# Kernel optimization log

Hardware: AMD Instinct MI355X
Metric: run time of the kernel (lower is better)

## Reference

```python
import jax, jax.numpy as jnp
import numpy as np

B, T, C, H = 4, 2048, 1024, 16
HD = C // H  # head dim = 64


def setup_inputs() -> dict:
    key = jax.random.key(0)
    ks = jax.random.split(key, 8)
    s = 1.0 / np.sqrt(C)
    return {
        "x": jax.random.normal(ks[0], (B, T, C), dtype=jnp.float32),
        "Wq": jax.random.normal(ks[1], (C, C), dtype=jnp.float32) * s,
        "bq": jax.random.normal(ks[2], (C,), dtype=jnp.float32) * 0.02,
        "Wk": jax.random.normal(ks[3], (C, C), dtype=jnp.float32) * s,
        "bk": jax.random.normal(ks[4], (C,), dtype=jnp.float32) * 0.02,
        "Wv": jax.random.normal(ks[5], (C, C), dtype=jnp.float32) * s,
        "bv": jax.random.normal(ks[6], (C,), dtype=jnp.float32) * 0.02,
        "Wp": jax.random.normal(ks[7], (C, C), dtype=jnp.float32) * s,
    }


def reference(x, Wq, bq, Wk, bk, Wv, bv, Wp):
    # Separate Q/K/V projections (torch Linear: y = x @ W.T + b)
    q = jnp.einsum("btc,dc->btd", x, Wq) + bq
    k = jnp.einsum("btc,dc->btd", x, Wk) + bk
    v = jnp.einsum("btc,dc->btd", x, Wv) + bv
    # split heads -> [B, H, T, HD]
    q = q.reshape(B, T, H, HD).transpose(0, 2, 1, 3)
    k = k.reshape(B, T, H, HD).transpose(0, 2, 1, 3)
    v = v.reshape(B, T, H, HD).transpose(0, 2, 1, 3)
    # causal scaled dot-product attention
    scale = 1.0 / np.sqrt(HD)
    scores = jnp.einsum("bhqd,bhkd->bhqk", q, k) * scale
    causal_mask = jnp.tril(jnp.ones((T, T), dtype=bool))  # [T, T]
    scores = jnp.where(causal_mask, scores, jnp.finfo(scores.dtype).min)
    att = jax.nn.softmax(scores, axis=-1)
    y = jnp.einsum("bhqk,bhkd->bhqd", att, v)
    # merge heads and output projection (no bias)
    y = y.transpose(0, 2, 1, 3).reshape(B, T, C)
    return jnp.einsum("btc,dc->btd", y, Wp)
```

## Files before the change

### kernel.cpp

```cpp
#include <hip/hip_runtime.h>
#include <stdint.h>


typedef unsigned short u16;
typedef short bf16x8 __attribute__((ext_vector_type(8)));
typedef float f32x4  __attribute__((ext_vector_type(4)));

#define LOG2E 1.4426950408889634f
#define CSHIFT 8.0f

__device__ __forceinline__ void gload_lds16(const void* g, void* l) {
  __builtin_amdgcn_global_load_lds(
      (const __attribute__((address_space(1))) void*)g,
      (__attribute__((address_space(3))) void*)l,
      16, 0, 0);
}

__device__ __forceinline__ u16 f2bf(float f) {
  union { float f; uint32_t u; } v; v.f = f;
  uint32_t u = v.u;
  u += 0x7fffu + ((u >> 16) & 1u);
  return (u16)(u >> 16);
}

__device__ __forceinline__ uint32_t pack_bf16(float a, float b) {
#if __has_builtin(__builtin_amdgcn_cvt_pk_bf16_f32)
  typedef short v2s __attribute__((ext_vector_type(2)));
  v2s r = __builtin_amdgcn_cvt_pk_bf16_f32(a, b);
  union { v2s s; uint32_t u; } c; c.s = r;
  return c.u;
#else
  return (uint32_t)f2bf(a) | ((uint32_t)f2bf(b) << 16);
#endif
}

__device__ __forceinline__ float fexp2(float x) {
#if __has_builtin(__builtin_amdgcn_exp2f)
  return __builtin_amdgcn_exp2f(x);
#else
  return exp2f(x);
#endif
}

__global__ void cvt_all_kernel(const float* __restrict__ x,
                               const float* __restrict__ w0,
                               const float* __restrict__ w1,
                               const float* __restrict__ w2,
                               const float* __restrict__ w3,
                               uint4* __restrict__ out) {
  int i = blockIdx.x * blockDim.x + threadIdx.x;
  if (i >= 1572864) return;
  const float* src;
  int local;
  if (i < 1048576) { src = x; local = i; }
  else {
    int j = i - 1048576;
    int seg = j >> 17;
    local = j & 131071;
    src = (seg == 0) ? w0 : (seg == 1) ? w1 : (seg == 2) ? w2 : w3;
  }
  const int blk = local >> 9, s = local & 511;
  const int tile = blk >> 5, ks = blk & 31;
  const int r = s >> 6, ln = s & 63;
  const int row = tile * 128 + r * 16 + (ln & 15);
  const int col = ks * 32 + (ln >> 4) * 8;
  const float4* p = (const float4*)(src + (size_t)row * 1024 + col);
  const float4 v0 = p[0], v1 = p[1];
  uint4 pk;
  pk.x = pack_bf16(v0.x, v0.y); pk.y = pack_bf16(v0.z, v0.w);
  pk.z = pack_bf16(v1.x, v1.y); pk.w = pack_bf16(v1.z, v1.w);
  out[i] = pk;
}

__global__ __launch_bounds__(256, 3) void gemm_qkv(
    const u16* __restrict__ A,
    const u16* __restrict__ Wq, const u16* __restrict__ Wk, const u16* __restrict__ Wv,
    const float* __restrict__ bq, const float* __restrict__ bk, const float* __restrict__ bv,
    u16* __restrict__ Qo, u16* __restrict__ Ko, u16* __restrict__ Vo) {
  __shared__ __attribute__((aligned(16))) u16 ldsA[3][4096];
  __shared__ __attribute__((aligned(16))) u16 ldsB[3][4096];
  const int tid = threadIdx.x;
  const int wv = tid >> 6, lane = tid & 63;
  const int cl = lane & 15, quad = lane >> 4;
  const int m0 = blockIdx.x * 128;
  const int mat = blockIdx.y >> 3;
  const int nt0 = blockIdx.y & 7;
  const int n0 = nt0 * 128;
  const int wm = (wv >> 1) * 64, wn = (wv & 1) * 64;
  const u16* W = (mat == 0) ? Wq : (mat == 1) ? Wk : Wv;
  const float* bias = (mat == 0) ? bq : (mat == 1) ? bk : bv;

  const u16* Abase = A + ((size_t)blockIdx.x << 17);
  const u16* Wbase = W + ((size_t)nt0 << 17);

  auto stage = [&](int buf, int ks) {
    const u16* a = Abase + ((size_t)ks << 12);
    const u16* w = Wbase + ((size_t)ks << 12);
    gload_lds16(a + tid * 8,        &ldsA[buf][tid * 8]);
    gload_lds16(a + 2048 + tid * 8, &ldsA[buf][2048 + tid * 8]);
    gload_lds16(w + tid * 8,        &ldsB[buf][tid * 8]);
    gload_lds16(w + 2048 + tid * 8, &ldsB[buf][2048 + tid * 8]);
  };

  f32x4 acc[4][4] = {};

  stage(0, 0);
  stage(1, 1);

  for (int kt = 0; kt < 32; ++kt) {
    if (kt < 31) {
      asm volatile("s_waitcnt vmcnt(4)" ::: "memory");
    } else {
      asm volatile("s_waitcnt vmcnt(0)" ::: "memory");
    }
    __builtin_amdgcn_s_barrier();
    if (kt < 30) stage((kt + 2) % 3, kt + 2);
    const int buf = kt % 3;
    bf16x8 af[4], bfr[4];
#pragma unroll
    for (int i = 0; i < 4; i++)
      af[i] = *(const bf16x8*)&ldsA[buf][(((wm >> 4) + i) * 64 + lane) * 8];
#pragma unroll
    for (int j = 0; j < 4; j++)
      bfr[j] = *(const bf16x8*)&ldsB[buf][(((wn >> 4) + j) * 64 + lane) * 8];
#pragma unroll
    for (int i = 0; i < 4; i++)
#pragma unroll
      for (int j = 0; j < 4; j++)
        acc[i][j] = __builtin_amdgcn_mfma_f32_16x16x32_bf16(af[i], bfr[j], acc[i][j], 0, 0, 0);
  }

  if (mat == 2) {
#pragma unroll
    for (int j = 0; j < 4; j++) {
      const int n = n0 + wn + j * 16 + cl;
      const float bj = bias[n];
      const int h = n >> 6, hd = n & 63;
#pragma unroll
      for (int i = 0; i < 4; i++) {
        const int m = m0 + wm + i * 16 + quad * 4;
        const int b = m >> 11, t = m & 2047;
        uint2 pk;
        pk.x = pack_bf16(acc[i][j][0] + bj, acc[i][j][1] + bj);
        pk.y = pack_bf16(acc[i][j][2] + bj, acc[i][j][3] + bj);
        const size_t off = ((size_t)(b * 16 + h) << 17) + ((size_t)(t >> 7) << 13)
                         + (size_t)(((hd >> 4) * 4 + ((t >> 5) & 3)) * 512
                                    + (((t >> 3) & 3) * 16 + (hd & 15)) * 8 + (t & 7));
        *(uint2*)(Vo + off) = pk;
      }
    }
  } else if (mat == 1) {
#pragma unroll
    for (int j = 0; j < 4; j++) {
      const int n = n0 + wn + j * 16 + cl;
      const float bj = bias[n];
      const int h = n >> 6, hd = n & 63;
      const int rlo = hd >> 5, lhi = ((hd >> 3) & 3) * 16, e = hd & 7;
#pragma unroll
      for (int i = 0; i < 4; i++) {
#pragma unroll
        for (int r = 0; r < 4; r++) {
          const int m = m0 + wm + i * 16 + quad * 4 + r;
          const int b = m >> 11, t = m & 2047;
          const size_t off = ((size_t)(b * 16 + h) << 17) + ((size_t)(t >> 7) << 13)
                           + (size_t)(((((t >> 4) & 7) * 2 + rlo) * 512)
                                      + (lhi + (t & 15)) * 8 + e);
          Ko[off] = f2bf(acc[i][j][r] + bj);
        }
      }
    }
  } else {
    const float sc = 0.125f * LOG2E;
#pragma unroll
    for (int j = 0; j < 4; j++) {
      const int n = n0 + wn + j * 16 + cl;
      const float bj = bias[n];
      const int h = n >> 6, hd = n & 63;
#pragma unroll
      for (int i = 0; i < 4; i++) {
#pragma unroll
        for (int r = 0; r < 4; r++) {
          const int m = m0 + wm + i * 16 + quad * 4 + r;
          const int b = m >> 11, t = m & 2047;
          Qo[((size_t)(b * 16 + h) * 2048 + t) * 64 + hd] = f2bf((acc[i][j][r] + bj) * sc);
        }
      }
    }
  }
}

__global__ __launch_bounds__(256, 3) void gemm_out(
    const u16* __restrict__ A, const u16* __restrict__ W,
    float* __restrict__ out) {
  __shared__ __attribute__((aligned(16))) u16 ldsA[3][4096];
  __shared__ __attribute__((aligned(16))) u16 ldsB[3][4096];
  const int tid = threadIdx.x;
  const int wv = tid >> 6, lane = tid & 63;
  const int cl = lane & 15, quad = lane >> 4;
  const int m0 = blockIdx.x * 128;
  const int n0 = blockIdx.y * 128;
  const int wm = (wv >> 1) * 64, wn = (wv & 1) * 64;

  const u16* Abase = A + ((size_t)blockIdx.x << 17);
  const u16* Wbase = W + ((size_t)blockIdx.y << 17);

  auto stage = [&](int buf, int ks) {
    const u16* a = Abase + ((size_t)ks << 12);
    const u16* w = Wbase + ((size_t)ks << 12);
    gload_lds16(a + tid * 8,        &ldsA[buf][tid * 8]);
    gload_lds16(a + 2048 + tid * 8, &ldsA[buf][2048 + tid * 8]);
    gload_lds16(w + tid * 8,        &ldsB[buf][tid * 8]);
    gload_lds16(w + 2048 + tid * 8, &ldsB[buf][2048 + tid * 8]);
  };

  f32x4 acc[4][4] = {};

  stage(0, 0);
  stage(1, 1);

  for (int kt = 0; kt < 32; ++kt) {
    if (kt < 31) {
      asm volatile("s_waitcnt vmcnt(4)" ::: "memory");
    } else {
      asm volatile("s_waitcnt vmcnt(0)" ::: "memory");
    }
    __builtin_amdgcn_s_barrier();
    if (kt < 30) stage((kt + 2) % 3, kt + 2);
    const int buf = kt % 3;
    bf16x8 af[4], bfr[4];
#pragma unroll
    for (int i = 0; i < 4; i++)
      af[i] = *(const bf16x8*)&ldsA[buf][(((wm >> 4) + i) * 64 + lane) * 8];
#pragma unroll
    for (int j = 0; j < 4; j++)
      bfr[j] = *(const bf16x8*)&ldsB[buf][(((wn >> 4) + j) * 64 + lane) * 8];
#pragma unroll
    for (int i = 0; i < 4; i++)
#pragma unroll
      for (int j = 0; j < 4; j++)
        acc[i][j] = __builtin_amdgcn_mfma_f32_16x16x32_bf16(af[i], bfr[j], acc[i][j], 0, 0, 0);
  }

#pragma unroll
  for (int j = 0; j < 4; j++) {
    const int n = n0 + wn + j * 16 + cl;
#pragma unroll
    for (int i = 0; i < 4; i++)
#pragma unroll
      for (int r = 0; r < 4; r++) {
        const int m = m0 + wm + i * 16 + quad * 4 + r;
        out[(size_t)m * 1024 + n] = acc[i][j][r];
      }
  }
}

__global__ __launch_bounds__(256, 2) void attn_kernel(
    const u16* __restrict__ Qb, const u16* __restrict__ Kb,
    const u16* __restrict__ Vtb, u16* __restrict__ Yb) {
  __shared__ __attribute__((aligned(16))) u16 ldsK[2][8192];
  __shared__ __attribute__((aligned(16))) u16 ldsV[8192];
  __shared__ __attribute__((aligned(16))) u16 ldsP[4][32][128];
  const int tid = threadIdx.x;
  const int wv = tid >> 6, lane = tid & 63;
  const int cl = lane & 15, quad = lane >> 4;
  const int p = blockIdx.x + (blockIdx.y << 3);
  const int xcd = p & 7, l = p >> 3;
  const int bh = xcd * 8 + (l & 7);
  const int qtb = l >> 3;
  const int qhi = 15 - qtb, qlo = qtb;
  const u16* Qh = Qb + (size_t)bh * 2048 * 64;
  const u16* Kh = Kb + ((size_t)bh << 17);
  const u16* Vh = Vtb + ((size_t)bh << 17);

  bf16x8 qf[2][2][2];
#pragma unroll
  for (int t = 0; t < 2; ++t) {
    const int q0 = (t == 0 ? qhi : qlo) * 128;
#pragma unroll
    for (int rt = 0; rt < 2; ++rt)
#pragma unroll
      for (int ks = 0; ks < 2; ++ks)
        qf[t][rt][ks] = *(const bf16x8*)&Qh[(size_t)(q0 + wv * 32 + rt * 16 + cl) * 64 + ks * 32 + quad * 8];
  }

  f32x4 o[2][2][4] = {};
  float ls[2][2] = {};

  auto stageK = [&](int buf, int kt) {
    const u16* kb2 = Kh + ((size_t)kt << 13);
#pragma unroll
    for (int rep = 0; rep < 4; ++rep)
      gload_lds16(kb2 + (rep * 256 + tid) * 8, &ldsK[buf][(rep * 256 + tid) * 8]);
  };
  auto stageV = [&](int kt) {
    const u16* vb2 = Vh + ((size_t)kt << 13);
#pragma unroll
    for (int rep = 0; rep < 4; ++rep)
      gload_lds16(vb2 + (rep * 256 + tid) * 8, &ldsV[(rep * 256 + tid) * 8]);
  };

  stageK(0, 0);

  for (int kt = 0; kt <= qhi; ++kt) {
    const int buf = kt & 1;
    const bool dolo = (kt <= qlo);
    __syncthreads();

    stageV(kt);

#pragma unroll
    for (int ct = 0; ct < 8; ++ct) {
      const bf16x8 kf0 = *(const bf16x8*)&ldsK[buf][((ct * 2 + 0) * 64 + lane) * 8];
      const bf16x8 kf1 = *(const bf16x8*)&ldsK[buf][((ct * 2 + 1) * 64 + lane) * 8];
#pragma unroll
      for (int rt = 0; rt < 2; ++rt) {
        f32x4 s = {};
        s = __builtin_amdgcn_mfma_f32_16x16x32_bf16(kf0, qf[0][rt][0], s, 0, 0, 0);
        s = __builtin_amdgcn_mfma_f32_16x16x32_bf16(kf1, qf[0][rt][1], s, 0, 0, 0);
        float pv[4];
#pragma unroll
        for (int r = 0; r < 4; ++r) {
          pv[r] = fexp2(s[r] - CSHIFT);
          if (kt == qhi) {
            if (ct * 16 + quad * 4 + r > wv * 32 + rt * 16 + cl) pv[r] = 0.f;
          }
          ls[0][rt] += pv[r];
        }
        const int rl = rt * 16 + cl;
        const int swch = (2 * ct + (quad >> 1)) ^ (cl & 7);
        uint2 pw;
        pw.x = pack_bf16(pv[0], pv[1]);
        pw.y = pack_bf16(pv[2], pv[3]);
        *(uint2*)&ldsP[wv][rl][(swch << 3) + (quad & 1) * 4] = pw;
      }
    }

    __syncthreads();

    if (kt < qhi) stageK(1 - buf, kt + 1);

#pragma unroll
    for (int ks = 0; ks < 4; ++ks) {
      bf16x8 pf[2];
#pragma unroll
      for (int rt = 0; rt < 2; ++rt)
        pf[rt] = *(const bf16x8*)&ldsP[wv][rt * 16 + cl][(((4 * ks + quad) ^ (cl & 7)) << 3)];
#pragma unroll
      for (int nt = 0; nt < 4; ++nt) {
        const bf16x8 vf = *(const bf16x8*)&ldsV[((nt * 4 + ks) * 64 + lane) * 8];
        o[0][0][nt] = __builtin_amdgcn_mfma_f32_16x16x32_bf16(pf[0], vf, o[0][0][nt], 0, 0, 0);
        o[0][1][nt] = __builtin_amdgcn_mfma_f32_16x16x32_bf16(pf[1], vf, o[0][1][nt], 0, 0, 0);
      }
    }

    if (dolo) {
#pragma unroll
      for (int ct = 0; ct < 8; ++ct) {
        const bf16x8 kf0 = *(const bf16x8*)&ldsK[buf][((ct * 2 + 0) * 64 + lane) * 8];
        const bf16x8 kf1 = *(const bf16x8*)&ldsK[buf][((ct * 2 + 1) * 64 + lane) * 8];
#pragma unroll
        for (int rt = 0; rt < 2; ++rt) {
          f32x4 s = {};
          s = __builtin_amdgcn_mfma_f32_16x16x32_bf16(kf0, qf[1][rt][0], s, 0, 0, 0);
          s = __builtin_amdgcn_mfma_f32_16x16x32_bf16(kf1, qf[1][rt][1], s, 0, 0, 0);
          float pv[4];
#pragma unroll
          for (int r = 0; r < 4; ++r) {
            pv[r] = fexp2(s[r] - CSHIFT);
            if (kt == qlo) {
              if (ct * 16 + quad * 4 + r > wv * 32 + rt * 16 + cl) pv[r] = 0.f;
            }
            ls[1][rt] += pv[r];
          }
          const int rl = rt * 16 + cl;
          const int swch = (2 * ct + (quad >> 1)) ^ (cl & 7);
          uint2 pw;
          pw.x = pack_bf16(pv[0], pv[1]);
          pw.y = pack_bf16(pv[2], pv[3]);
          *(uint2*)&ldsP[wv][rl][(swch << 3) + (quad & 1) * 4] = pw;
        }
      }
#pragma unroll
      for (int ks = 0; ks < 4; ++ks) {
        bf16x8 pf[2];
#pragma unroll
        for (int rt = 0; rt < 2; ++rt)
          pf[rt] = *(const bf16x8*)&ldsP[wv][rt * 16 + cl][(((4 * ks + quad) ^ (cl & 7)) << 3)];
#pragma unroll
        for (int nt = 0; nt < 4; ++nt) {
          const bf16x8 vf = *(const bf16x8*)&ldsV[((nt * 4 + ks) * 64 + lane) * 8];
          o[1][0][nt] = __builtin_amdgcn_mfma_f32_16x16x32_bf16(pf[0], vf, o[1][0][nt], 0, 0, 0);
          o[1][1][nt] = __builtin_amdgcn_mfma_f32_16x16x32_bf16(pf[1], vf, o[1][1][nt], 0, 0, 0);
        }
      }
    }
  }

  const int bb = bh >> 4, h = bh & 15;
#pragma unroll
  for (int t = 0; t < 2; ++t) {
    const int q0 = (t == 0 ? qhi : qlo) * 128;
#pragma unroll
    for (int rt = 0; rt < 2; ++rt) {
      float s = ls[t][rt];
      s += __shfl_xor(s, 16, 64);
      s += __shfl_xor(s, 32, 64);
#pragma unroll
      for (int r = 0; r < 4; ++r) {
        const float inv = 1.0f / __shfl(s, quad * 4 + r, 64);
        const int q = q0 + wv * 32 + rt * 16 + quad * 4 + r;
        const int row = bb * 2048 + q;
#pragma unroll
        for (int nt = 0; nt < 4; ++nt) {
          const int col = h * 64 + nt * 16 + cl;
          const size_t off = ((size_t)((row >> 7) * 32 + (col >> 5)) << 12)
                           + (size_t)((((row >> 4) & 7) * 64 + ((col >> 3) & 3) * 16 + (row & 15)) * 8
                                      + (col & 7));
          Yb[off] = f2bf(o[t][rt][nt][r] * inv);
        }
      }
    }
  }
}

extern "C" void kernel_launch(void* const* d_in, const int* in_sizes, int n_in,
                              void* d_out, int out_size, void* d_ws, size_t ws_size,
                              hipStream_t stream) {
  const float* x  = (const float*)d_in[0];
  const float* Wq = (const float*)d_in[1];
  const float* bq = (const float*)d_in[2];
  const float* Wk = (const float*)d_in[3];
  const float* bk = (const float*)d_in[4];
  const float* Wv = (const float*)d_in[5];
  const float* bv = (const float*)d_in[6];
  const float* Wp = (const float*)d_in[7];

  u16* xb  = (u16*)d_ws;
  u16* wqb = xb  + 8388608;
  u16* wkb = wqb + 1048576;
  u16* wvb = wkb + 1048576;
  u16* wpb = wvb + 1048576;
  u16* Qb  = wpb + 1048576;
  u16* Kb  = Qb  + 8388608;
  u16* Vtb = Kb  + 8388608;
  u16* Yb  = Vtb + 8388608;

  cvt_all_kernel<<<6144, 256, 0, stream>>>(x, Wq, Wk, Wv, Wp, (uint4*)d_ws);

  gemm_qkv<<<dim3(64, 24), 256, 0, stream>>>(xb, wqb, wkb, wvb, bq, bk, bv,
                                             Qb, Kb, Vtb);

  attn_kernel<<<dim3(8, 64), 256, 0, stream>>>(Qb, Kb, Vtb, Yb);

  gemm_out<<<dim3(64, 8), 256, 0, stream>>>(Yb, wpb, (float*)d_out);
}
```

Before: 246.5 us.

## Stage GEMM epilogues through LDS and compute softmax row sums via MFMA

The QKV and output GEMM epilogues now write accumulators into a reused shared-memory tile and then emit coalesced 16-byte global stores, replacing scattered 2- and 4-byte stores. In attention, the per-lane softmax denominator accumulation and cross-lane shuffles are replaced by an extra MFMA against a ones vector, with a fast reciprocal for the final normalization. This trades extra LDS traffic, barriers and MFMA work for fewer VALU ops and better store coalescing.

```diff
diff --git a/kernel.cpp b/kernel.cpp
--- a/kernel.cpp
+++ b/kernel.cpp
@@ -39,6 +39,14 @@
   return __builtin_amdgcn_exp2f(x);
 #else
   return exp2f(x);
+#endif
+}
+
+__device__ __forceinline__ float frcp(float x) {
+#if __has_builtin(__builtin_amdgcn_rcpf)
+  return __builtin_amdgcn_rcpf(x);
+#else
+  return 1.0f / x;
 #endif
 }
 
@@ -77,8 +85,7 @@
     const u16* __restrict__ Wq, const u16* __restrict__ Wk, const u16* __restrict__ Wv,
     const float* __restrict__ bq, const float* __restrict__ bk, const float* __restrict__ bv,
     u16* __restrict__ Qo, u16* __restrict__ Ko, u16* __restrict__ Vo) {
-  __shared__ __attribute__((aligned(16))) u16 ldsA[3][4096];
-  __shared__ __attribute__((aligned(16))) u16 ldsB[3][4096];
+  __shared__ __attribute__((aligned(16))) u16 shm[24576];
   const int tid = threadIdx.x;
   const int wv = tid >> 6, lane = tid & 63;
   const int cl = lane & 15, quad = lane >> 4;
@@ -96,10 +103,12 @@
   auto stage = [&](int buf, int ks) {
     const u16* a = Abase + ((size_t)ks << 12);
     const u16* w = Wbase + ((size_t)ks << 12);
-    gload_lds16(a + tid * 8,        &ldsA[buf][tid * 8]);
-    gload_lds16(a + 2048 + tid * 8, &ldsA[buf][2048 + tid * 8]);
-    gload_lds16(w + tid * 8,        &ldsB[buf][tid * 8]);
-    gload_lds16(w + 2048 + tid * 8, &ldsB[buf][2048 + tid * 8]);
+    u16* la = &shm[buf * 4096];
+    u16* lb = &shm[12288 + buf * 4096];
+    gload_lds16(a + tid * 8,        la + tid * 8);
+    gload_lds16(a + 2048 + tid * 8, la + 2048 + tid * 8);
+    gload_lds16(w + tid * 8,        lb + tid * 8);
+    gload_lds16(w + 2048 + tid * 8, lb + 2048 + tid * 8);
   };
 
   f32x4 acc[4][4] = {};
@@ -116,13 +125,15 @@
     __builtin_amdgcn_s_barrier();
     if (kt < 30) stage((kt + 2) % 3, kt + 2);
     const int buf = kt % 3;
+    const u16* la = &shm[buf * 4096];
+    const u16* lb = &shm[12288 + buf * 4096];
     bf16x8 af[4], bfr[4];
 #pragma unroll
     for (int i = 0; i < 4; i++)
-      af[i] = *(const bf16x8*)&ldsA[buf][(((wm >> 4) + i) * 64 + lane) * 8];
+      af[i] = *(const bf16x8*)&la[(((wm >> 4) + i) * 64 + lane) * 8];
 #pragma unroll
     for (int j = 0; j < 4; j++)
-      bfr[j] = *(const bf16x8*)&ldsB[buf][(((wn >> 4) + j) * 64 + lane) * 8];
+      bfr[j] = *(const bf16x8*)&lb[(((wn >> 4) + j) * 64 + lane) * 8];
 #pragma unroll
     for (int i = 0; i < 4; i++)
 #pragma unroll
@@ -130,42 +141,40 @@
         acc[i][j] = __builtin_amdgcn_mfma_f32_16x16x32_bf16(af[i], bfr[j], acc[i][j], 0, 0, 0);
   }
 
+  __syncthreads();
+  u16* etile = shm;
+
   if (mat == 2) {
 #pragma unroll
     for (int j = 0; j < 4; j++) {
-      const int n = n0 + wn + j * 16 + cl;
-      const float bj = bias[n];
-      const int h = n >> 6, hd = n & 63;
+      const int n_loc = wn + j * 16 + cl;
+      const float bj = bias[n0 + n_loc];
+      const int hh = n_loc >> 6, hd = n_loc & 63;
 #pragma unroll
       for (int i = 0; i < 4; i++) {
-        const int m = m0 + wm + i * 16 + quad * 4;
-        const int b = m >> 11, t = m & 2047;
+        const int tb = wm + i * 16 + quad * 4;
         uint2 pk;
         pk.x = pack_bf16(acc[i][j][0] + bj, acc[i][j][1] + bj);
         pk.y = pack_bf16(acc[i][j][2] + bj, acc[i][j][3] + bj);
-        const size_t off = ((size_t)(b * 16 + h) << 17) + ((size_t)(t >> 7) << 13)
-                         + (size_t)(((hd >> 4) * 4 + ((t >> 5) & 3)) * 512
-                                    + (((t >> 3) & 3) * 16 + (hd & 15)) * 8 + (t & 7));
-        *(uint2*)(Vo + off) = pk;
+        const int off = ((hd >> 4) * 4 + ((tb >> 5) & 3)) * 512
+                      + (((tb >> 3) & 3) * 16 + (hd & 15)) * 8 + (tb & 7);
+        *(uint2*)&etile[hh * 8192 + off] = pk;
       }
     }
   } else if (mat == 1) {
 #pragma unroll
     for (int j = 0; j < 4; j++) {
-      const int n = n0 + wn + j * 16 + cl;
-      const float bj = bias[n];
-      const int h = n >> 6, hd = n & 63;
+      const int n_loc = wn + j * 16 + cl;
+      const float bj = bias[n0 + n_loc];
+      const int hh = n_loc >> 6, hd = n_loc & 63;
       const int rlo = hd >> 5, lhi = ((hd >> 3) & 3) * 16, e = hd & 7;
 #pragma unroll
       for (int i = 0; i < 4; i++) {
 #pragma unroll
         for (int r = 0; r < 4; r++) {
-          const int m = m0 + wm + i * 16 + quad * 4 + r;
-          const int b = m >> 11, t = m & 2047;
-          const size_t off = ((size_t)(b * 16 + h) << 17) + ((size_t)(t >> 7) << 13)
-                           + (size_t)(((((t >> 4) & 7) * 2 + rlo) * 512)
-                                      + (lhi + (t & 15)) * 8 + e);
-          Ko[off] = f2bf(acc[i][j][r] + bj);
+          const int tl = wm + i * 16 + quad * 4 + r;
+          const int off = (((tl >> 4) & 7) * 2 + rlo) * 512 + (lhi + (tl & 15)) * 8 + e;
+          etile[hh * 8192 + off] = f2bf(acc[i][j][r] + bj);
         }
       }
     }
@@ -173,18 +182,40 @@
     const float sc = 0.125f * LOG2E;
 #pragma unroll
     for (int j = 0; j < 4; j++) {
-      const int n = n0 + wn + j * 16 + cl;
-      const float bj = bias[n];
-      const int h = n >> 6, hd = n & 63;
+      const int n_loc = wn + j * 16 + cl;
+      const float bj = bias[n0 + n_loc];
+      const int hh = n_loc >> 6, hd = n_loc & 63;
 #pragma unroll
       for (int i = 0; i < 4; i++) {
 #pragma unroll
         for (int r = 0; r < 4; r++) {
-          const int m = m0 + wm + i * 16 + quad * 4 + r;
-          const int b = m >> 11, t = m & 2047;
-          Qo[((size_t)(b * 16 + h) * 2048 + t) * 64 + hd] = f2bf((acc[i][j][r] + bj) * sc);
+          const int tl = wm + i * 16 + quad * 4 + r;
+          etile[hh * 8192 + tl * 64 + hd] = f2bf((acc[i][j][r] + bj) * sc);
         }
       }
+    }
+  }
+  __syncthreads();
+
+  const int b = m0 >> 11, t0 = m0 & 2047;
+  const int h0 = n0 >> 6;
+  if (mat == 0) {
+#pragma unroll
+    for (int p = 0; p < 8; ++p) {
+      const int idx = p * 2048 + tid * 8;
+      const int hh = idx >> 13, off = idx & 8191;
+      u16* dst = Qo + ((size_t)(b * 16 + h0 + hh) * 2048 + t0) * 64 + off;
+      *(uint4*)dst = *(const uint4*)&etile[idx];
+    }
+  } else {
+    u16* base = (mat == 1) ? Ko : Vo;
+    const int kt = t0 >> 7;
+#pragma unroll
+    for (int p = 0; p < 8; ++p) {
+      const int idx = p * 2048 + tid * 8;
+      const int hh = idx >> 13, off = idx & 8191;
+      u16* dst = base + ((size_t)(b * 16 + h0 + hh) << 17) + ((size_t)kt << 13) + off;
+      *(uint4*)dst = *(const uint4*)&etile[idx];
     }
   }
 }
@@ -192,8 +223,7 @@
 __global__ __launch_bounds__(256, 3) void gemm_out(
     const u16* __restrict__ A, const u16* __restrict__ W,
     float* __restrict__ out) {
-  __shared__ __attribute__((aligned(16))) u16 ldsA[3][4096];
-  __shared__ __attribute__((aligned(16))) u16 ldsB[3][4096];
+  __shared__ __attribute__((aligned(16))) u16 shm[24576];
   const int tid = threadIdx.x;
   const int wv = tid >> 6, lane = tid & 63;
   const int cl = lane & 15, quad = lane >> 4;
@@ -207,10 +237,12 @@
   auto stage = [&](int buf, int ks) {
     const u16* a = Abase + ((size_t)ks << 12);
     const u16* w = Wbase + ((size_t)ks << 12);
-    gload_lds16(a + tid * 8,        &ldsA[buf][tid * 8]);
-    gload_lds16(a + 2048 + tid * 8, &ldsA[buf][2048 + tid * 8]);
-    gload_lds16(w + tid * 8,        &ldsB[buf][tid * 8]);
-    gload_lds16(w + 2048 + tid * 8, &ldsB[buf][2048 + tid * 8]);
+    u16* la = &shm[buf * 4096];
+    u16* lb = &shm[12288 + buf * 4096];
+    gload_lds16(a + tid * 8,        la + tid * 8);
+    gload_lds16(a + 2048 + tid * 8, la + 2048 + tid * 8);
+    gload_lds16(w + tid * 8,        lb + tid * 8);
+    gload_lds16(w + 2048 + tid * 8, lb + 2048 + tid * 8);
   };
 
   f32x4 acc[4][4] = {};
@@ -227,13 +259,15 @@
     __builtin_amdgcn_s_barrier();
     if (kt < 30) stage((kt + 2) % 3, kt + 2);
     const int buf = kt % 3;
+    const u16* la = &shm[buf * 4096];
+    const u16* lb = &shm[12288 + buf * 4096];
     bf16x8 af[4], bfr[4];
 #pragma unroll
     for (int i = 0; i < 4; i++)
-      af[i] = *(const bf16x8*)&ldsA[buf][(((wm >> 4) + i) * 64 + lane) * 8];
+      af[i] = *(const bf16x8*)&la[(((wm >> 4) + i) * 64 + lane) * 8];
 #pragma unroll
     for (int j = 0; j < 4; j++)
-      bfr[j] = *(const bf16x8*)&ldsB[buf][(((wn >> 4) + j) * 64 + lane) * 8];
+      bfr[j] = *(const bf16x8*)&lb[(((wn >> 4) + j) * 64 + lane) * 8];
 #pragma unroll
     for (int i = 0; i < 4; i++)
 #pragma unroll
@@ -241,16 +275,33 @@
         acc[i][j] = __builtin_amdgcn_mfma_f32_16x16x32_bf16(af[i], bfr[j], acc[i][j], 0, 0, 0);
   }
 
-#pragma unroll
-  for (int j = 0; j < 4; j++) {
-    const int n = n0 + wn + j * 16 + cl;
-#pragma unroll
-    for (int i = 0; i < 4; i++)
-#pragma unroll
-      for (int r = 0; r < 4; r++) {
-        const int m = m0 + wm + i * 16 + quad * 4 + r;
-        out[(size_t)m * 1024 + n] = acc[i][j][r];
-      }
+  __syncthreads();
+  float* etf = (float*)shm;
+#pragma unroll
+  for (int p = 0; p < 2; ++p) {
+    if ((wm >> 6) == p) {
+#pragma unroll
+      for (int j = 0; j < 4; j++) {
+        const int col = wn + j * 16 + cl;
+#pragma unroll
+        for (int i = 0; i < 4; i++)
+#pragma unroll
+          for (int r = 0; r < 4; r++) {
+            const int row = i * 16 + quad * 4 + r;
+            etf[row * 128 + col] = acc[i][j][r];
+          }
+      }
+    }
+    __syncthreads();
+#pragma unroll
+    for (int c = 0; c < 8; ++c) {
+      const int lin4 = c * 256 + tid;
+      const int fidx = lin4 * 4;
+      const int row = fidx >> 7, col = fidx & 127;
+      *(float4*)(out + (size_t)(m0 + p * 64 + row) * 1024 + n0 + col) =
+          *(const float4*)&etf[fidx];
+    }
+    __syncthreads();
   }
 }
 
@@ -283,8 +334,15 @@
         qf[t][rt][ks] = *(const bf16x8*)&Qh[(size_t)(q0 + wv * 32 + rt * 16 + cl) * 64 + ks * 32 + quad * 8];
   }
 
+  bf16x8 vone;
+  {
+    const short ob = (short)0x3F80;
+#pragma unroll
+    for (int e = 0; e < 8; ++e) vone[e] = (cl == 0) ? ob : (short)0;
+  }
+
   f32x4 o[2][2][4] = {};
-  float ls[2][2] = {};
+  f32x4 osum[2][2] = {};
 
   auto stageK = [&](int buf, int kt) {
     const u16* kb2 = Kh + ((size_t)kt << 13);
@@ -324,7 +382,6 @@
           if (kt == qhi) {
             if (ct * 16 + quad * 4 + r > wv * 32 + rt * 16 + cl) pv[r] = 0.f;
           }
-          ls[0][rt] += pv[r];
         }
         const int rl = rt * 16 + cl;
         const int swch = (2 * ct + (quad >> 1)) ^ (cl & 7);
@@ -351,6 +408,8 @@
         o[0][0][nt] = __builtin_amdgcn_mfma_f32_16x16x32_bf16(pf[0], vf, o[0][0][nt], 0, 0, 0);
         o[0][1][nt] = __builtin_amdgcn_mfma_f32_16x16x32_bf16(pf[1], vf, o[0][1][nt], 0, 0, 0);
       }
+      osum[0][0] = __builtin_amdgcn_mfma_f32_16x16x32_bf16(pf[0], vone, osum[0][0], 0, 0, 0);
+      osum[0][1] = __builtin_amdgcn_mfma_f32_16x16x32_bf16(pf[1], vone, osum[0][1], 0, 0, 0);
     }
 
     if (dolo) {
@@ -370,7 +429,6 @@
             if (kt == qlo) {
               if (ct * 16 + quad * 4 + r > wv * 32 + rt * 16 + cl) pv[r] = 0.f;
             }
-            ls[1][rt] += pv[r];
           }
           const int rl = rt * 16 + cl;
           const int swch = (2 * ct + (quad >> 1)) ^ (cl & 7);
@@ -392,6 +450,8 @@
           o[1][0][nt] = __builtin_amdgcn_mfma_f32_16x16x32_bf16(pf[0], vf, o[1][0][nt], 0, 0, 0);
           o[1][1][nt] = __builtin_amdgcn_mfma_f32_16x16x32_bf16(pf[1], vf, o[1][1][nt], 0, 0, 0);
         }
+        osum[1][0] = __builtin_amdgcn_mfma_f32_16x16x32_bf16(pf[0], vone, osum[1][0], 0, 0, 0);
+        osum[1][1] = __builtin_amdgcn_mfma_f32_16x16x32_bf16(pf[1], vone, osum[1][1], 0, 0, 0);
       }
     }
   }
@@ -402,12 +462,10 @@
     const int q0 = (t == 0 ? qhi : qlo) * 128;
 #pragma unroll
     for (int rt = 0; rt < 2; ++rt) {
-      float s = ls[t][rt];
-      s += __shfl_xor(s, 16, 64);
-      s += __shfl_xor(s, 32, 64);
 #pragma unroll
       for (int r = 0; r < 4; ++r) {
-        const float inv = 1.0f / __shfl(s, quad * 4 + r, 64);
+        const float den = __shfl(osum[t][rt][r], quad << 4, 64);
+        const float inv = frcp(den);
         const int q = q0 + wv * 32 + rt * 16 + quad * 4 + r;
         const int row = bb * 2048 + q;
 #pragma unroll
```

Result: no change. 243.2 us (-1.3%).
